# Performance work log

Hardware: AMD Instinct MI355X
Metric: run time of the kernel (lower is better)

The kernel has to match this reference:

```python
import jax, jax.numpy as jnp
import numpy as np
from jax import lax

B = 64
FEAT = 512
SEED_DIM = 128
NUM_PC = 256
NPART = 4096
NFPS = 512


def setup_inputs() -> dict:
    key = jax.random.key(0)
    ks = jax.random.split(key, 32)
    s = 0.02
    rn = lambda k, shape: jax.random.normal(k, shape, jnp.float32) * s
    inp = {}
    inp["feat"] = jax.random.normal(ks[0], (B, FEAT, 1), jnp.float32)
    inp["patch_xyz"] = jax.random.normal(ks[1], (B, 3, 128), jnp.float32)
    inp["patch_feat"] = jax.random.normal(ks[2], (B, FEAT, 128), jnp.float32)
    inp["partial"] = jax.random.normal(ks[3], (B, NPART, 3), jnp.float32)
    # ConvTranspose1d(512, 128, 256): weight [in, out, k]
    inp["ps_w"] = rn(ks[4], (FEAT, 128, NUM_PC))
    inp["ps_b"] = jnp.zeros((128,), jnp.float32)
    # MLP_Res(in, hidden, out): conv1 [hid,in], conv2 [out,hid], shortcut [out,in]
    def mlp_res_params(k, din, dhid, dout):
        k1, k2, k3 = jax.random.split(k, 3)
        return (rn(k1, (dhid, din)), jnp.zeros((dhid,), jnp.float32),
                rn(k2, (dout, dhid)), jnp.zeros((dout,), jnp.float32),
                rn(k3, (dout, din)), jnp.zeros((dout,), jnp.float32))
    (inp["m1_w1"], inp["m1_b1"], inp["m1_w2"], inp["m1_b2"], inp["m1_ws"], inp["m1_bs"]) = mlp_res_params(ks[5], FEAT + 128, 128, 128)
    (inp["m2_w1"], inp["m2_b1"], inp["m2_w2"], inp["m2_b2"], inp["m2_ws"], inp["m2_bs"]) = mlp_res_params(ks[6], 128, 64, 128)
    (inp["m3_w1"], inp["m3_b1"], inp["m3_w2"], inp["m3_b2"], inp["m3_ws"], inp["m3_bs"]) = mlp_res_params(ks[7], FEAT + 128, 128, SEED_DIM)
    inp["m4_w1"] = rn(ks[8], (64, SEED_DIM))
    inp["m4_b1"] = jnp.zeros((64,), jnp.float32)
    inp["m4_w2"] = rn(ks[9], (3, 64))
    inp["m4_b2"] = jnp.zeros((3,), jnp.float32)
    return inp


def _conv1(w, b, x):
    # 1x1 Conv1d: w [out,in], x [B,in,N] -> [B,out,N]
    return jnp.einsum('oi,bin->bon', w, x) + b[None, :, None]


def _mlp_res(x, w1, b1, w2, b2, ws, bs):
    h = jax.nn.relu(_conv1(w1, b1, x))
    return _conv1(w2, b2, h) + _conv1(ws, bs, x)


def _fps(xyz, npoint):
    # farthest point sampling (PointNet++ semantics, start at index 0)
    # xyz: [B, N, 3] -> [B, npoint, 3]
    Bb, N, _ = xyz.shape
    dist0 = jnp.full((Bb, N), 1e10, dtype=xyz.dtype)
    far0 = jnp.zeros((Bb,), jnp.int32)

    def step(carry, _):
        dist, far = carry
        centroid = jnp.take_along_axis(xyz, far[:, None, None], axis=1)  # [B,1,3]
        d = jnp.sum((xyz - centroid) ** 2, axis=-1)  # [B,N]
        dist = jnp.minimum(dist, d)
        new_far = jnp.argmax(dist, axis=-1).astype(jnp.int32)
        return (dist, new_far), far

    _, idxs = lax.scan(step, (dist0, far0), None, length=npoint)  # [npoint, B]
    idxs = idxs.T  # [B, npoint]
    return jnp.take_along_axis(xyz, idxs[..., None], axis=1)


def reference(feat, patch_xyz, patch_feat, partial,
              ps_w, ps_b,
              m1_w1, m1_b1, m1_w2, m1_b2, m1_ws, m1_bs,
              m2_w1, m2_b1, m2_w2, m2_b2, m2_ws, m2_bs,
              m3_w1, m3_b1, m3_w2, m3_b2, m3_ws, m3_bs,
              m4_w1, m4_b1, m4_w2, m4_b2):
    # ConvTranspose1d on length-1 input: [B,C,1] x [C,O,K] -> [B,O,K]
    x1 = jnp.einsum('bc,cok->bok', feat[:, :, 0], ps_w) + ps_b[None, :, None]
    feat_r = jnp.broadcast_to(feat, (feat.shape[0], feat.shape[1], NUM_PC))
    x1 = _mlp_res(jnp.concatenate([x1, feat_r], axis=1), m1_w1, m1_b1, m1_w2, m1_b2, m1_ws, m1_bs)
    x2 = _mlp_res(x1, m2_w1, m2_b1, m2_w2, m2_b2, m2_ws, m2_bs)
    x3 = _mlp_res(jnp.concatenate([x2, feat_r], axis=1), m3_w1, m3_b1, m3_w2, m3_b2, m3_ws, m3_bs)
    seed = _conv1(m4_w2, m4_b2, jax.nn.relu(_conv1(m4_w1, m4_b1, x3)))  # [B,3,256]
    all_pts = jnp.concatenate([seed.transpose(0, 2, 1), partial], axis=1)  # [B,256+N,3]
    x = _fps(all_pts, NFPS).transpose(0, 2, 1)  # [B,3,512]
    return (seed, x3, x)
```

## Files before the change

### kernel.cpp

```cpp
#include <hip/hip_runtime.h>
#include <stdint.h>

#define X3_OFF 49152
#define FPS_OFF 2146304


typedef float v2f __attribute__((ext_vector_type(2)));

__global__ void k_prep(const float* __restrict__ feat, float* __restrict__ ws) {
    int g = blockIdx.x * 256 + threadIdx.x;
    int c = g >> 6, b = g & 63;
    ws[32768 + c * 64 + b] = feat[b * 512 + c];
}

__global__ void k_tterms(const float* __restrict__ w1, const float* __restrict__ ws1,
                         const float* __restrict__ w3, const float* __restrict__ ws3,
                         float* __restrict__ ws) {
    int g = blockIdx.x * 256 + threadIdx.x;
    int which = g >> 13;
    int o = (g >> 6) & 127;
    int b = g & 63;
    const float* W = (which == 0) ? w1 : (which == 1) ? ws1
                     : (which == 2) ? w3 : ws3;
    const float* ft = ws + 32768;
    float acc = 0.f;
    for (int c = 0; c < 512; ++c)
        acc = fmaf(W[o * 640 + 128 + c], ft[c * 64 + b], acc);
    ws[which * 8192 + o * 64 + b] = acc;
}

__global__ void k_deconv(const float* __restrict__ psw,
                         const float* __restrict__ psb,
                         const float* __restrict__ ws,
                         float* __restrict__ stage) {
    int n = blockIdx.x * 256 + threadIdx.x;
    int b0 = blockIdx.y * 16;
    const float* featT = ws + 32768;
    float acc[16];
    float bias = psb[n >> 8];
#pragma unroll
    for (int j = 0; j < 16; ++j) acc[j] = bias;
    for (int c = 0; c < 512; ++c) {
        float pw = psw[c * 32768 + n];
#pragma unroll
        for (int j = 0; j < 16; ++j)
            acc[j] = fmaf(pw, featT[c * 64 + b0 + j], acc[j]);
    }
#pragma unroll
    for (int j = 0; j < 16; ++j)
        stage[(b0 + j) * 32768 + n] = acc[j];
}

__device__ __forceinline__ void gemm8(const float* __restrict__ Wg, int ld, int o0,
                                      const float* S, int K, float acc[8], int lane) {
#pragma unroll 4
    for (int i = 0; i < K; ++i) {
        float x = S[i * 64 + lane];
#pragma unroll
        for (int r = 0; r < 8; ++r)
            acc[r] = fmaf(x, Wg[(o0 + r) * ld + i], acc[r]);
    }
}

struct FusedW {
    const float *m1_w1, *m1_b1, *m1_w2, *m1_b2, *m1_ws, *m1_bs;
    const float *m2_w1, *m2_b1, *m2_w2, *m2_b2, *m2_ws, *m2_bs;
    const float *m3_w1, *m3_b1, *m3_w2, *m3_b2, *m3_ws, *m3_bs;
    const float *m4_w1, *m4_b1, *m4_w2, *m4_b2;
};

__global__ void __launch_bounds__(512)
k_fused(FusedW P, const float* __restrict__ ws, float* __restrict__ fout) {
    int b  = blockIdx.x >> 2;
    int k0 = (blockIdx.x & 3) * 64;
    int lane = threadIdx.x & 63;
    int wave = __builtin_amdgcn_readfirstlane(threadIdx.x >> 6);

    const float* T1  = ws;
    const float* T1s = ws + 8192;
    const float* T3  = ws + 16384;
    const float* T3s = ws + 24576;
    float* stage = fout + X3_OFF + b * 32768;

    __shared__ float Xs[8192];
    __shared__ float Hs[8192];

#pragma unroll
    for (int s = 0; s < 16; ++s) {
        int e = threadIdx.x + s * 512;
        int o = e >> 6, kk = e & 63;
        Xs[e] = stage[o * 256 + k0 + kk];
    }
    __syncthreads();

    float yreg[2][8];

#pragma unroll
    for (int half = 0; half < 2; ++half) {
        int o0 = wave * 16 + half * 8;
        float acc[8];
#pragma unroll
        for (int r = 0; r < 8; ++r) acc[r] = T1[(o0 + r) * 64 + b] + P.m1_b1[o0 + r];
        gemm8(P.m1_w1, 640, o0, Xs, 128, acc, lane);
#pragma unroll
        for (int r = 0; r < 8; ++r) Hs[(o0 + r) * 64 + lane] = fmaxf(acc[r], 0.f);
    }
    __syncthreads();
#pragma unroll
    for (int half = 0; half < 2; ++half) {
        int o0 = wave * 16 + half * 8;
        float acc[8];
#pragma unroll
        for (int r = 0; r < 8; ++r)
            acc[r] = T1s[(o0 + r) * 64 + b] + P.m1_b2[o0 + r] + P.m1_bs[o0 + r];
        gemm8(P.m1_w2, 128, o0, Hs, 128, acc, lane);
        gemm8(P.m1_ws, 640, o0, Xs, 128, acc, lane);
#pragma unroll
        for (int r = 0; r < 8; ++r) yreg[half][r] = acc[r];
    }
    __syncthreads();
#pragma unroll
    for (int half = 0; half < 2; ++half) {
        int o0 = wave * 16 + half * 8;
#pragma unroll
        for (int r = 0; r < 8; ++r) Xs[(o0 + r) * 64 + lane] = yreg[half][r];
    }
    __syncthreads();

    {
        int o0 = wave * 8;
        float acc[8];
#pragma unroll
        for (int r = 0; r < 8; ++r) acc[r] = P.m2_b1[o0 + r];
        gemm8(P.m2_w1, 128, o0, Xs, 128, acc, lane);
#pragma unroll
        for (int r = 0; r < 8; ++r) Hs[(o0 + r) * 64 + lane] = fmaxf(acc[r], 0.f);
    }
    __syncthreads();
#pragma unroll
    for (int half = 0; half < 2; ++half) {
        int o0 = wave * 16 + half * 8;
        float acc[8];
#pragma unroll
        for (int r = 0; r < 8; ++r) acc[r] = P.m2_b2[o0 + r] + P.m2_bs[o0 + r];
        gemm8(P.m2_w2, 64, o0, Hs, 64, acc, lane);
        gemm8(P.m2_ws, 128, o0, Xs, 128, acc, lane);
#pragma unroll
        for (int r = 0; r < 8; ++r) yreg[half][r] = acc[r];
    }
    __syncthreads();
#pragma unroll
    for (int half = 0; half < 2; ++half) {
        int o0 = wave * 16 + half * 8;
#pragma unroll
        for (int r = 0; r < 8; ++r) Xs[(o0 + r) * 64 + lane] = yreg[half][r];
    }
    __syncthreads();

#pragma unroll
    for (int half = 0; half < 2; ++half) {
        int o0 = wave * 16 + half * 8;
        float acc[8];
#pragma unroll
        for (int r = 0; r < 8; ++r) acc[r] = T3[(o0 + r) * 64 + b] + P.m3_b1[o0 + r];
        gemm8(P.m3_w1, 640, o0, Xs, 128, acc, lane);
#pragma unroll
        for (int r = 0; r < 8; ++r) Hs[(o0 + r) * 64 + lane] = fmaxf(acc[r], 0.f);
    }
    __syncthreads();
#pragma unroll
    for (int half = 0; half < 2; ++half) {
        int o0 = wave * 16 + half * 8;
        float acc[8];
#pragma unroll
        for (int r = 0; r < 8; ++r)
            acc[r] = T3s[(o0 + r) * 64 + b] + P.m3_b2[o0 + r] + P.m3_bs[o0 + r];
        gemm8(P.m3_w2, 128, o0, Hs, 128, acc, lane);
        gemm8(P.m3_ws, 640, o0, Xs, 128, acc, lane);
#pragma unroll
        for (int r = 0; r < 8; ++r) yreg[half][r] = acc[r];
    }
    __syncthreads();
#pragma unroll
    for (int half = 0; half < 2; ++half) {
        int o0 = wave * 16 + half * 8;
#pragma unroll
        for (int r = 0; r < 8; ++r) {
            Xs[(o0 + r) * 64 + lane] = yreg[half][r];
            stage[(o0 + r) * 256 + k0 + lane] = yreg[half][r];
        }
    }
    __syncthreads();

    {
        int o0 = wave * 8;
        float acc[8];
#pragma unroll
        for (int r = 0; r < 8; ++r) acc[r] = P.m4_b1[o0 + r];
        gemm8(P.m4_w1, 128, o0, Xs, 128, acc, lane);
#pragma unroll
        for (int r = 0; r < 8; ++r) Hs[(o0 + r) * 64 + lane] = fmaxf(acc[r], 0.f);
    }
    __syncthreads();
    if (wave < 3) {
        int d = wave;
        float s = P.m4_b2[d];
        for (int j = 0; j < 64; ++j)
            s = fmaf(Hs[j * 64 + lane], P.m4_w2[d * 64 + j], s);
        fout[b * 768 + d * 256 + k0 + lane] = s;
    }
}

__device__ __forceinline__ unsigned wave_max_u32_l63(unsigned v) {
    unsigned t;
    t = (unsigned)__builtin_amdgcn_update_dpp(0, (int)v, 0x111, 0xf, 0xf, false); v = t > v ? t : v;
    t = (unsigned)__builtin_amdgcn_update_dpp(0, (int)v, 0x112, 0xf, 0xf, false); v = t > v ? t : v;
    t = (unsigned)__builtin_amdgcn_update_dpp(0, (int)v, 0x114, 0xf, 0xf, false); v = t > v ? t : v;
    t = (unsigned)__builtin_amdgcn_update_dpp(0, (int)v, 0x118, 0xf, 0xf, false); v = t > v ? t : v;
    t = (unsigned)__builtin_amdgcn_update_dpp(0, (int)v, 0x142, 0xa, 0xf, false); v = t > v ? t : v;
    t = (unsigned)__builtin_amdgcn_update_dpp(0, (int)v, 0x143, 0xc, 0xf, false); v = t > v ? t : v;
    return v;
}
__device__ __forceinline__ unsigned wave_min_u32_l63(unsigned v) {
    unsigned t;
    t = (unsigned)__builtin_amdgcn_update_dpp(-1, (int)v, 0x111, 0xf, 0xf, false); v = t < v ? t : v;
    t = (unsigned)__builtin_amdgcn_update_dpp(-1, (int)v, 0x112, 0xf, 0xf, false); v = t < v ? t : v;
    t = (unsigned)__builtin_amdgcn_update_dpp(-1, (int)v, 0x114, 0xf, 0xf, false); v = t < v ? t : v;
    t = (unsigned)__builtin_amdgcn_update_dpp(-1, (int)v, 0x118, 0xf, 0xf, false); v = t < v ? t : v;
    t = (unsigned)__builtin_amdgcn_update_dpp(-1, (int)v, 0x142, 0xa, 0xf, false); v = t < v ? t : v;
    t = (unsigned)__builtin_amdgcn_update_dpp(-1, (int)v, 0x143, 0xc, 0xf, false); v = t < v ? t : v;
    return v;
}

__global__ void __launch_bounds__(256)
k_fps(const float* __restrict__ seed, const float* __restrict__ partial,
      float* __restrict__ outx) {
#pragma clang fp contract(off)
    int b = blockIdx.x;
    int tid = threadIdx.x;
    int lane = tid & 63;
    int wv = tid >> 6;

    __shared__ float pts[4352 * 3];
    __shared__ unsigned long long cand[2][4];
    __shared__ int fars[512];

    pts[tid * 3 + 0] = seed[b * 768 + tid];
    pts[tid * 3 + 1] = seed[b * 768 + 256 + tid];
    pts[tid * 3 + 2] = seed[b * 768 + 512 + tid];
#pragma unroll
    for (int j = 0; j < 48; ++j) {
        int e = tid + j * 256;
        pts[768 + e] = partial[b * 12288 + e];
    }
    if (tid == 0) fars[0] = 0;
    __syncthreads();

    v2f px2[8], py2[8], pz2[8], d2[8];
#pragma unroll
    for (int k = 0; k < 8; ++k) {
        int g0 = (2 * k) * 256 + tid;
        int g1 = g0 + 256;
        px2[k] = (v2f){pts[g0 * 3 + 0], pts[g1 * 3 + 0]};
        py2[k] = (v2f){pts[g0 * 3 + 1], pts[g1 * 3 + 1]};
        pz2[k] = (v2f){pts[g0 * 3 + 2], pts[g1 * 3 + 2]};
        d2[k] = (v2f){1e10f, 1e10f};
    }
    float px1, py1, pz1, d1;
    {
        int g = 16 * 256 + tid;
        px1 = pts[g * 3 + 0];
        py1 = pts[g * 3 + 1];
        pz1 = pts[g * 3 + 2];
        d1 = 1e10f;
    }
    float cx = pts[0], cy = pts[1], cz = pts[2];

    for (int t = 0; t < 511; ++t) {
        float bv = -1.0f; int bg = 0;
#pragma unroll
        for (int k = 0; k < 8; ++k) {
            v2f dx = px2[k] - cx;
            v2f dy = py2[k] - cy;
            v2f dz = pz2[k] - cz;
            v2f dd = (dx * dx + dy * dy) + dz * dz;
            float n0 = fminf(d2[k].x, dd.x);
            float n1 = fminf(d2[k].y, dd.y);
            d2[k] = (v2f){n0, n1};
            if (n0 > bv) { bv = n0; bg = (2 * k) * 256 + tid; }
            if (n1 > bv) { bv = n1; bg = (2 * k + 1) * 256 + tid; }
        }
        {
            float dx = px1 - cx, dy = py1 - cy, dz = pz1 - cz;
            float dd = (dx * dx + dy * dy) + dz * dz;
            d1 = fminf(d1, dd);
            if (d1 > bv) { bv = d1; bg = 16 * 256 + tid; }
        }
        unsigned mv = wave_max_u32_l63(__float_as_uint(bv));
        unsigned maxbits = (unsigned)__builtin_amdgcn_readlane((int)mv, 63);
        unsigned cg = (__float_as_uint(bv) == maxbits) ? (unsigned)bg : 0xFFFFFFFFu;
        unsigned mgv = wave_min_u32_l63(cg);
        unsigned big = (unsigned)__builtin_amdgcn_readlane((int)mgv, 63);

        if (lane == 0)
            cand[t & 1][wv] = (((unsigned long long)maxbits) << 32) |
                              (unsigned long long)(8191u - big);
        __syncthreads();
        unsigned long long U0 = cand[t & 1][0];
        unsigned long long U1 = cand[t & 1][1];
        unsigned long long U2 = cand[t & 1][2];
        unsigned long long U3 = cand[t & 1][3];
        if (U1 > U0) U0 = U1;
        if (U3 > U2) U2 = U3;
        if (U2 > U0) U0 = U2;
        int bi = 8191 - (int)(U0 & 8191ull);
        cx = pts[bi * 3 + 0]; cy = pts[bi * 3 + 1]; cz = pts[bi * 3 + 2];
        if (tid == 0) fars[t + 1] = bi;
    }
    __syncthreads();

#pragma unroll
    for (int j = 0; j < 2; ++j) {
        int n = tid + j * 256;
        int idx = fars[n];
        int ob = b * 1536 + n;
        outx[ob]        = pts[idx * 3 + 0];
        outx[ob + 512]  = pts[idx * 3 + 1];
        outx[ob + 1024] = pts[idx * 3 + 2];
    }
}

extern "C" void kernel_launch(void* const* d_in, const int* in_sizes, int n_in,
                              void* d_out, int out_size, void* d_ws, size_t ws_size,
                              hipStream_t stream) {
    (void)in_sizes; (void)n_in; (void)out_size; (void)ws_size;
    const float* feat    = (const float*)d_in[0];
    const float* partial = (const float*)d_in[3];
    const float* psw     = (const float*)d_in[4];
    const float* psb     = (const float*)d_in[5];

    FusedW P;
    P.m1_w1 = (const float*)d_in[6];  P.m1_b1 = (const float*)d_in[7];
    P.m1_w2 = (const float*)d_in[8];  P.m1_b2 = (const float*)d_in[9];
    P.m1_ws = (const float*)d_in[10]; P.m1_bs = (const float*)d_in[11];
    P.m2_w1 = (const float*)d_in[12]; P.m2_b1 = (const float*)d_in[13];
    P.m2_w2 = (const float*)d_in[14]; P.m2_b2 = (const float*)d_in[15];
    P.m2_ws = (const float*)d_in[16]; P.m2_bs = (const float*)d_in[17];
    P.m3_w1 = (const float*)d_in[18]; P.m3_b1 = (const float*)d_in[19];
    P.m3_w2 = (const float*)d_in[20]; P.m3_b2 = (const float*)d_in[21];
    P.m3_ws = (const float*)d_in[22]; P.m3_bs = (const float*)d_in[23];
    P.m4_w1 = (const float*)d_in[24]; P.m4_b1 = (const float*)d_in[25];
    P.m4_w2 = (const float*)d_in[26]; P.m4_b2 = (const float*)d_in[27];

    float* W = (float*)d_ws;
    float* out = (float*)d_out;

    k_prep<<<dim3(128), dim3(256), 0, stream>>>(feat, W);
    k_tterms<<<dim3(128), dim3(256), 0, stream>>>(P.m1_w1, P.m1_ws, P.m3_w1, P.m3_ws, W);
    k_deconv<<<dim3(128, 4), dim3(256), 0, stream>>>(psw, psb, W, out + X3_OFF);
    k_fused<<<dim3(256), dim3(512), 0, stream>>>(P, W, out);
    k_fps<<<dim3(64), dim3(256), 0, stream>>>(out, partial, out + FPS_OFF);
}
```

Before: 735.6 us.

## Restructure FPS inner loop: scalar distances, tree argmax, broadcast winner coordinates

Replaces the packed v2f distance updates with 17 scalar per-thread distances using explicit non-fused rounding. The serial compare-and-select argmax becomes a tree max followed by a tree min over slot indices. Each wave also publishes its candidate's xyz to shared memory, so the next centroid comes from the candidate buffer rather than a dependent indexed LDS load after the barrier. The aim is to shorten the serial dependency chain in each of the 511 iterations, at the cost of losing packed-math throughput and adding extra shared-memory writes and selects.

New measurement: 768.0 us. +4.4%, slower.

```diff
diff --git a/kernel.cpp b/kernel.cpp
--- a/kernel.cpp
+++ b/kernel.cpp
@@ -4,8 +4,6 @@
 #define X3_OFF 49152
 #define FPS_OFF 2146304
 
-
-typedef float v2f __attribute__((ext_vector_type(2)));
 
 __global__ void k_prep(const float* __restrict__ feat, float* __restrict__ ws) {
     int g = blockIdx.x * 256 + threadIdx.x;
@@ -232,10 +230,11 @@
     return v;
 }
 
+__device__ __forceinline__ unsigned umin_u(unsigned a, unsigned b) { return a < b ? a : b; }
+
 __global__ void __launch_bounds__(256)
 k_fps(const float* __restrict__ seed, const float* __restrict__ partial,
       float* __restrict__ outx) {
-#pragma clang fp contract(off)
     int b = blockIdx.x;
     int tid = threadIdx.x;
     int lane = tid & 63;
@@ -243,6 +242,7 @@
 
     __shared__ float pts[4352 * 3];
     __shared__ unsigned long long cand[2][4];
+    __shared__ float candxyz[2][4][3];
     __shared__ int fars[512];
 
     pts[tid * 3 + 0] = seed[b * 768 + tid];
@@ -256,66 +256,78 @@
     if (tid == 0) fars[0] = 0;
     __syncthreads();
 
-    v2f px2[8], py2[8], pz2[8], d2[8];
-#pragma unroll
-    for (int k = 0; k < 8; ++k) {
-        int g0 = (2 * k) * 256 + tid;
-        int g1 = g0 + 256;
-        px2[k] = (v2f){pts[g0 * 3 + 0], pts[g1 * 3 + 0]};
-        py2[k] = (v2f){pts[g0 * 3 + 1], pts[g1 * 3 + 1]};
-        pz2[k] = (v2f){pts[g0 * 3 + 2], pts[g1 * 3 + 2]};
-        d2[k] = (v2f){1e10f, 1e10f};
-    }
-    float px1, py1, pz1, d1;
-    {
-        int g = 16 * 256 + tid;
-        px1 = pts[g * 3 + 0];
-        py1 = pts[g * 3 + 1];
-        pz1 = pts[g * 3 + 2];
-        d1 = 1e10f;
+    float px[17], py[17], pz[17], dist[17];
+#pragma unroll
+    for (int s = 0; s < 17; ++s) {
+        int g = s * 256 + tid;
+        px[s] = pts[g * 3 + 0];
+        py[s] = pts[g * 3 + 1];
+        pz[s] = pts[g * 3 + 2];
+        dist[s] = 1e10f;
     }
     float cx = pts[0], cy = pts[1], cz = pts[2];
 
     for (int t = 0; t < 511; ++t) {
-        float bv = -1.0f; int bg = 0;
-#pragma unroll
-        for (int k = 0; k < 8; ++k) {
-            v2f dx = px2[k] - cx;
-            v2f dy = py2[k] - cy;
-            v2f dz = pz2[k] - cz;
-            v2f dd = (dx * dx + dy * dy) + dz * dz;
-            float n0 = fminf(d2[k].x, dd.x);
-            float n1 = fminf(d2[k].y, dd.y);
-            d2[k] = (v2f){n0, n1};
-            if (n0 > bv) { bv = n0; bg = (2 * k) * 256 + tid; }
-            if (n1 > bv) { bv = n1; bg = (2 * k + 1) * 256 + tid; }
+#pragma unroll
+        for (int s = 0; s < 17; ++s) {
+            float dx = px[s] - cx, dy = py[s] - cy, dz = pz[s] - cz;
+            float d = __fadd_rn(__fadd_rn(__fmul_rn(dx, dx), __fmul_rn(dy, dy)),
+                                __fmul_rn(dz, dz));
+            dist[s] = fminf(dist[s], d);
         }
-        {
-            float dx = px1 - cx, dy = py1 - cy, dz = pz1 - cz;
-            float dd = (dx * dx + dy * dy) + dz * dz;
-            d1 = fminf(d1, dd);
-            if (d1 > bv) { bv = d1; bg = 16 * 256 + tid; }
-        }
-        unsigned mv = wave_max_u32_l63(__float_as_uint(bv));
+        float a0 = fmaxf(fmaxf(dist[0], dist[1]), dist[2]);
+        float a1 = fmaxf(fmaxf(dist[3], dist[4]), dist[5]);
+        float a2 = fmaxf(fmaxf(dist[6], dist[7]), dist[8]);
+        float a3 = fmaxf(fmaxf(dist[9], dist[10]), dist[11]);
+        float a4 = fmaxf(fmaxf(dist[12], dist[13]), dist[14]);
+        float a5 = fmaxf(dist[15], dist[16]);
+        float b0 = fmaxf(fmaxf(a0, a1), a2);
+        float b1 = fmaxf(fmaxf(a3, a4), a5);
+        float m  = fmaxf(b0, b1);
+        unsigned e[17];
+#pragma unroll
+        for (int s = 0; s < 17; ++s)
+            e[s] = (dist[s] == m) ? (unsigned)s : 63u;
+        unsigned c0 = umin_u(umin_u(e[0], e[1]), e[2]);
+        unsigned c1 = umin_u(umin_u(e[3], e[4]), e[5]);
+        unsigned c2 = umin_u(umin_u(e[6], e[7]), e[8]);
+        unsigned c3 = umin_u(umin_u(e[9], e[10]), e[11]);
+        unsigned c4 = umin_u(umin_u(e[12], e[13]), e[14]);
+        unsigned c5 = umin_u(e[15], e[16]);
+        unsigned d0 = umin_u(umin_u(c0, c1), c2);
+        unsigned d1 = umin_u(umin_u(c3, c4), c5);
+        unsigned sm = umin_u(d0, d1);
+        unsigned bg = (sm << 8) + (unsigned)tid;
+
+        unsigned mv = wave_max_u32_l63(__float_as_uint(m));
         unsigned maxbits = (unsigned)__builtin_amdgcn_readlane((int)mv, 63);
-        unsigned cg = (__float_as_uint(bv) == maxbits) ? (unsigned)bg : 0xFFFFFFFFu;
+        unsigned cg = (__float_as_uint(m) == maxbits) ? bg : 0xFFFFFFFFu;
         unsigned mgv = wave_min_u32_l63(cg);
         unsigned big = (unsigned)__builtin_amdgcn_readlane((int)mgv, 63);
 
         if (lane == 0)
             cand[t & 1][wv] = (((unsigned long long)maxbits) << 32) |
                               (unsigned long long)(8191u - big);
+        if (lane < 3)
+            candxyz[t & 1][wv][lane] = pts[big * 3 + lane];
         __syncthreads();
+
         unsigned long long U0 = cand[t & 1][0];
         unsigned long long U1 = cand[t & 1][1];
         unsigned long long U2 = cand[t & 1][2];
         unsigned long long U3 = cand[t & 1][3];
-        if (U1 > U0) U0 = U1;
-        if (U3 > U2) U2 = U3;
-        if (U2 > U0) U0 = U2;
-        int bi = 8191 - (int)(U0 & 8191ull);
-        cx = pts[bi * 3 + 0]; cy = pts[bi * 3 + 1]; cz = pts[bi * 3 + 2];
-        if (tid == 0) fars[t + 1] = bi;
+        float x0 = candxyz[t & 1][0][0], y0 = candxyz[t & 1][0][1], z0 = candxyz[t & 1][0][2];
+        float x1 = candxyz[t & 1][1][0], y1 = candxyz[t & 1][1][1], z1 = candxyz[t & 1][1][2];
+        float x2 = candxyz[t & 1][2][0], y2 = candxyz[t & 1][2][1], z2 = candxyz[t & 1][2][2];
+        float x3 = candxyz[t & 1][3][0], y3 = candxyz[t & 1][3][1], z3 = candxyz[t & 1][3][2];
+        bool s1 = U1 > U0;
+        U0 = s1 ? U1 : U0; x0 = s1 ? x1 : x0; y0 = s1 ? y1 : y0; z0 = s1 ? z1 : z0;
+        bool s3 = U3 > U2;
+        U2 = s3 ? U3 : U2; x2 = s3 ? x3 : x2; y2 = s3 ? y3 : y2; z2 = s3 ? z3 : z2;
+        bool s2 = U2 > U0;
+        U0 = s2 ? U2 : U0; x0 = s2 ? x2 : x0; y0 = s2 ? y2 : y0; z0 = s2 ? z2 : z0;
+        cx = x0; cy = y0; cz = z0;
+        if (tid == 0) fars[t + 1] = 8191 - (int)(U0 & 8191ull);
     }
     __syncthreads();
 
```
